# Kernel tuning notes

Hardware: AMD Instinct MI355X
Metric: run time of the kernel (lower is better)

## Reference

```python
import jax, jax.numpy as jnp
import numpy as np

B, L, F_DIM, H = 4, 384, 640, 128
K_COULOMB = 332.0
DIELECTRIC = 80.0
BN_EPS = 1e-5

# amino-acid charge table, index order 'ACDEFGHIKLMNPQRSTVWY'
_AA = 'ACDEFGHIKLMNPQRSTVWY'
_CHG = {'D': -1.0, 'E': -1.0, 'K': 1.0, 'R': 1.0, 'H': 0.1}
_TABLE = np.zeros((20, 3), dtype=np.float32)
for _i, _aa in enumerate(_AA):
    c = _CHG.get(_aa, 0.0)
    _TABLE[_i, 0 if c > 0 else (1 if c < 0 else 2)] = 1.0
CHG_TABLE = jnp.asarray(_TABLE)


def _conv1d(x, w, b, pad):
    # x: [N, Cin, L], w: [Cout, Cin, K]
    y = jax.lax.conv_general_dilated(x, w, (1,), [(pad, pad)],
                                     dimension_numbers=('NCH', 'OIH', 'NCH'))
    return y + b[None, :, None]


def setup_inputs() -> dict:
    key = jax.random.key(0)
    ks = jax.random.split(key, 32)
    s = 0.05

    def rn(k, shape):
        return (jax.random.normal(k, shape) * s).astype(jnp.float32)

    inp = {
        'features': jax.random.normal(ks[0], (B, L, F_DIM), dtype=jnp.float32),
        'seq_ids': jax.random.randint(ks[1], (B, L), 0, 20, dtype=jnp.int32),
        'structures': (jax.random.normal(ks[2], (B, L, 3)) * 10.0).astype(jnp.float32),
        # charge predictor: Linear(F,H) -> ReLU -> BN(H) -> Linear(H,H//2) -> ReLU -> Linear(H//2,3) -> Softmax
        'W1': rn(ks[3], (F_DIM, H)), 'b1': jnp.zeros((H,), jnp.float32),
        'gamma': jnp.ones((H,), jnp.float32), 'beta': jnp.zeros((H,), jnp.float32),
        'rmean': jnp.zeros((H,), jnp.float32), 'rvar': jnp.ones((H,), jnp.float32),
        'W2': rn(ks[4], (H, H // 2)), 'b2': jnp.zeros((H // 2,), jnp.float32),
        'W3': rn(ks[5], (H // 2, 3)), 'b3': jnp.zeros((3,), jnp.float32),
        # salt bridge detector: Linear(2F+1,H) -> ReLU -> Linear(H,64) -> ReLU -> Linear(64,1) -> Sigmoid
        'sW1': rn(ks[6], (2 * F_DIM + 1, H)), 'sb1': jnp.zeros((H,), jnp.float32),
        'sW2': rn(ks[7], (H, 64)), 'sb2': jnp.zeros((64,), jnp.float32),
        'sW3': rn(ks[8], (64, 1)), 'sb3': jnp.zeros((1,), jnp.float32),
        # potential calculator convs (OIH layout)
        'c1w': rn(ks[9], (16, 1, 5)), 'c1b': jnp.zeros((16,), jnp.float32),
        'c2w': rn(ks[10], (8, 16, 3)), 'c2b': jnp.zeros((8,), jnp.float32),
        'c3w': rn(ks[11], (1, 8, 3)), 'c3b': jnp.zeros((1,), jnp.float32),
    }
    return inp


def reference(features, seq_ids, structures,
              W1, b1, gamma, beta, rmean, rvar, W2, b2, W3, b3,
              sW1, sb1, sW2, sb2, sW3, sb3,
              c1w, c1b, c2w, c2b, c3w, c3b):
    b_, l_, f_ = features.shape

    # true charges from sequence (one-hot pos/neg/neutral)
    true_charges = CHG_TABLE[seq_ids]                               # [B,L,3]

    # --- charge predictor (BatchNorm in eval mode: running stats) ---
    x = features.reshape(-1, f_)
    h = jax.nn.relu(x @ W1 + b1)
    h = gamma * (h - rmean) / jnp.sqrt(rvar + BN_EPS) + beta
    h = jax.nn.relu(h @ W2 + b2)
    pc = jax.nn.softmax(h @ W3 + b3, axis=-1).reshape(b_, l_, 3)    # [B,L,3]

    net_charge = pc[:, :, 0:1] - pc[:, :, 1:2]                      # [B,L,1]

    # --- electrostatic potential: 1D conv stack on [B,1,L] ---
    p = net_charge.transpose(0, 2, 1)                               # [B,1,L]
    p = jax.nn.relu(_conv1d(p, c1w, c1b, 2))
    p = jax.nn.relu(_conv1d(p, c2w, c2b, 1))
    p = _conv1d(p, c3w, c3b, 1)
    potential = p.transpose(0, 2, 1)                                # [B,L,1]

    # --- pairwise distances ---
    diff = structures[:, :, None, :] - structures[:, None, :, :]    # [B,L,L,3]
    D = jnp.sqrt(jnp.sum(diff * diff, axis=-1) + 1e-12)             # [B,L,L]

    # --- salt bridges: vectorized edge-MLP over all (pos i, neg j) pairs ---
    pos = pc[:, :, 0] > pc[:, :, 2]                                 # [B,L]
    neg = pc[:, :, 1] > pc[:, :, 2]                                 # [B,L]
    a, bb, d = sW1[:f_], sW1[f_:2 * f_], sW1[2 * f_]                # split cat([fi,fj,dist]) @ sW1
    fi = features @ a                                               # [B,L,H]
    fj = features @ bb                                              # [B,L,H]
    hid = jax.nn.relu(fi[:, :, None, :] + fj[:, None, :, :] + D[..., None] * d + sb1)  # [B,L,L,H]
    hid2 = jax.nn.relu(hid @ sW2 + sb2)                             # [B,L,L,64]
    prob = jax.nn.sigmoid((hid2 @ sW3 + sb3)[..., 0])               # [B,L,L]
    q = pos[:, :, None] & neg[:, None, :] & (D < 4.0) & (prob > 0.5)
    salt_bridge_masks = (q | q.transpose(0, 2, 1)).astype(jnp.float32)  # [B,L,L]

    # --- Coulomb energy with distance-dependent dielectric ---
    # dielectric = eps * D / 4 -> e_ij = k * q_i q_j / (eps/4 * D^2)
    qc = pc[:, :, 0] - pc[:, :, 1]                                  # [B,L]
    valid = (D < 15.0) & (D > 0.0)
    triu = jnp.triu(jnp.ones((l_, l_), bool), k=1)[None]
    D_safe = jnp.where(valid, D, 1.0)
    e_ij = K_COULOMB * qc[:, :, None] * qc[:, None, :] / ((DIELECTRIC / 4.0) * D_safe * D_safe)
    energy = jnp.sum(jnp.where(valid & triu, e_ij, 0.0), axis=(1, 2))  # [B]

    return (pc, true_charges, net_charge, potential, salt_bridge_masks, energy)
```

## Files before the change

### kernel.cpp

```cpp
#include <hip/hip_runtime.h>

#define LSEQ 384
#define NROWS 1536
#define FDIM 640
#define HDIM 128
#define PART 196608

#define WS_H1   0
#define WS_FI   393216
#define WS_FJ   786432
#define WS_QC   1179648
#define WS_FLAG 1181184
#define WS_CNT  1182720
#define WS_LIST 1182724
#define CAPMAX  65536

#define OUT_PC    0
#define OUT_TC    4608
#define OUT_NET   9216
#define OUT_POT   10752
#define OUT_MASK  12288
#define OUT_EN    602112

__global__ __launch_bounds__(256) void k_gemm(const float* __restrict__ X,
                                              const float* __restrict__ W1,
                                              const float* __restrict__ sW1,
                                              float* __restrict__ ws) {
    __shared__ float As[32][34];
    __shared__ float Bs[32][64];
    const int t  = threadIdx.x;
    const int m0 = blockIdx.x * 32;
    const int gy = blockIdx.y;
    const int kz = blockIdx.z;
    const int mat = gy >> 1, half = gy & 1, n0 = half * 64;
    const float* W = (mat == 0) ? W1 : (mat == 1 ? sW1 : sW1 + 640 * 128);
    float* O = ws + (mat == 0 ? WS_H1 : (mat == 1 ? WS_FI : WS_FJ)) + kz * PART;

    const int a_r = t >> 3;
    const int a_c = (t & 7) * 4;
    const int b_r = t >> 4;
    const int b_c = (t & 15) * 4;
    const int tx  = (t & 15) * 4;
    const int ty  = (t >> 4) * 2;

    float acc[2][4] = {};
    const int k0 = kz * 320;

    for (int kk = k0; kk < k0 + 320; kk += 32) {
        float4 av = *(const float4*)&X[(m0 + a_r) * FDIM + kk + a_c];
        As[a_c + 0][a_r] = av.x;
        As[a_c + 1][a_r] = av.y;
        As[a_c + 2][a_r] = av.z;
        As[a_c + 3][a_r] = av.w;
        *(float4*)&Bs[b_r][b_c]      = *(const float4*)&W[(kk + b_r) * HDIM + n0 + b_c];
        *(float4*)&Bs[b_r + 16][b_c] = *(const float4*)&W[(kk + b_r + 16) * HDIM + n0 + b_c];
        __syncthreads();
#pragma unroll
        for (int k = 0; k < 32; k++) {
            float2 a = *(const float2*)&As[k][ty];
            float4 b = *(const float4*)&Bs[k][tx];
            acc[0][0] = fmaf(a.x, b.x, acc[0][0]);
            acc[0][1] = fmaf(a.x, b.y, acc[0][1]);
            acc[0][2] = fmaf(a.x, b.z, acc[0][2]);
            acc[0][3] = fmaf(a.x, b.w, acc[0][3]);
            acc[1][0] = fmaf(a.y, b.x, acc[1][0]);
            acc[1][1] = fmaf(a.y, b.y, acc[1][1]);
            acc[1][2] = fmaf(a.y, b.z, acc[1][2]);
            acc[1][3] = fmaf(a.y, b.w, acc[1][3]);
        }
        __syncthreads();
    }
#pragma unroll
    for (int r = 0; r < 2; r++) {
        float4 v = make_float4(acc[r][0], acc[r][1], acc[r][2], acc[r][3]);
        *(float4*)&O[(m0 + ty + r) * HDIM + n0 + tx] = v;
    }
}

__global__ __launch_bounds__(256) void k_row(const float* __restrict__ h1a,
                                             const float* __restrict__ h1b,
                                             const float* __restrict__ b1,
                                             const float* __restrict__ gam,
                                             const float* __restrict__ bet,
                                             const float* __restrict__ rmean,
                                             const float* __restrict__ rvar,
                                             const float* __restrict__ W2,
                                             const float* __restrict__ b2,
                                             const float* __restrict__ W3,
                                             const float* __restrict__ b3,
                                             const int* __restrict__ seq,
                                             float* __restrict__ out,
                                             float* __restrict__ qc,
                                             int* __restrict__ flags) {
    __shared__ float sh[4][130];
    const int t = threadIdx.x, w = t >> 6, lane = t & 63;
    const int row = blockIdx.x * 4 + w;
#pragma unroll
    for (int c = lane; c < 128; c += 64) {
        float v = h1a[row * HDIM + c] + h1b[row * HDIM + c] + b1[c];
        v = fmaxf(v, 0.0f);
        v = gam[c] * (v - rmean[c]) / sqrtf(rvar[c] + 1e-5f) + bet[c];
        sh[w][c] = v;
    }
    __syncthreads();
    float acc = b2[lane];
#pragma unroll 8
    for (int c = 0; c < 128; c++)
        acc = fmaf(sh[w][c], W2[c * 64 + lane], acc);
    float h2 = fmaxf(acc, 0.0f);
    float x0 = h2 * W3[lane * 3 + 0];
    float x1 = h2 * W3[lane * 3 + 1];
    float x2 = h2 * W3[lane * 3 + 2];
#pragma unroll
    for (int o = 32; o > 0; o >>= 1) {
        x0 += __shfl_xor(x0, o, 64);
        x1 += __shfl_xor(x1, o, 64);
        x2 += __shfl_xor(x2, o, 64);
    }
    if (lane == 0) {
        float l0 = x0 + b3[0], l1 = x1 + b3[1], l2 = x2 + b3[2];
        float m = fmaxf(l0, fmaxf(l1, l2));
        float e0 = expf(l0 - m), e1 = expf(l1 - m), e2 = expf(l2 - m);
        float s = e0 + e1 + e2;
        float pc0 = e0 / s, pc1 = e1 / s, pc2 = e2 / s;
        out[OUT_PC + row * 3 + 0] = pc0;
        out[OUT_PC + row * 3 + 1] = pc1;
        out[OUT_PC + row * 3 + 2] = pc2;
        float net = pc0 - pc1;
        out[OUT_NET + row] = net;
        qc[row] = net;
        flags[row] = (pc0 > pc2 ? 1 : 0) | (pc1 > pc2 ? 2 : 0);
        int sid = seq[row];
        float c0 = (sid == 6 || sid == 8 || sid == 14) ? 1.0f : 0.0f;
        float c1 = (sid == 2 || sid == 3) ? 1.0f : 0.0f;
        out[OUT_TC + row * 3 + 0] = c0;
        out[OUT_TC + row * 3 + 1] = c1;
        out[OUT_TC + row * 3 + 2] = (c0 == 0.0f && c1 == 0.0f) ? 1.0f : 0.0f;
    }
}

__global__ __launch_bounds__(384) void k_conv(const float* __restrict__ net,
                                              const float* __restrict__ c1w, const float* __restrict__ c1b,
                                              const float* __restrict__ c2w, const float* __restrict__ c2b,
                                              const float* __restrict__ c3w, const float* __restrict__ c3b,
                                              float* __restrict__ out,
                                              unsigned int* __restrict__ cnt) {
    __shared__ float p0[LSEQ + 4];
    __shared__ float p1[16][LSEQ + 2];
    __shared__ float p2[8][LSEQ + 2];
    const int b = blockIdx.x, t = threadIdx.x;
    p0[t + 2] = net[b * LSEQ + t];
    if (t < 2) { p0[t] = 0.0f; p0[LSEQ + 2 + t] = 0.0f; }
    if (t < 16) { p1[t][0] = 0.0f; p1[t][LSEQ + 1] = 0.0f; }
    if (t < 8)  { p2[t][0] = 0.0f; p2[t][LSEQ + 1] = 0.0f; }
    if (b == 0) {
        if (t < 4) out[OUT_EN + t] = 0.0f;
        if (t == 4) *cnt = 0u;
    }
    __syncthreads();
#pragma unroll
    for (int o = 0; o < 16; o++) {
        float acc = c1b[o];
#pragma unroll
        for (int k = 0; k < 5; k++) acc = fmaf(p0[t + k], c1w[o * 5 + k], acc);
        p1[o][t + 1] = fmaxf(acc, 0.0f);
    }
    __syncthreads();
#pragma unroll
    for (int o = 0; o < 8; o++) {
        float acc = c2b[o];
        for (int i = 0; i < 16; i++)
#pragma unroll
            for (int k = 0; k < 3; k++)
                acc = fmaf(p1[i][t + k], c2w[(o * 16 + i) * 3 + k], acc);
        p2[o][t + 1] = fmaxf(acc, 0.0f);
    }
    __syncthreads();
    {
        float acc = c3b[0];
        for (int i = 0; i < 8; i++)
#pragma unroll
            for (int k = 0; k < 3; k++)
                acc = fmaf(p2[i][t + k], c3w[i * 3 + k], acc);
        out[OUT_POT + b * LSEQ + t] = acc;
    }
}

__global__ __launch_bounds__(256) void k_pair(const float* __restrict__ S,
                                              const float* __restrict__ qc,
                                              const int* __restrict__ flags,
                                              float* __restrict__ out,
                                              unsigned int* __restrict__ cnt,
                                              unsigned int* __restrict__ list,
                                              unsigned int cap) {
    __shared__ float sx[LSEQ], sy[LSEQ], sz[LSEQ], sq[LSEQ];
    __shared__ int sf[LSEQ];
    __shared__ float red[4];
    const int row = blockIdx.x;
    const int b = row / LSEQ;
    const int i = row - b * LSEQ;
    const int t = threadIdx.x;
    for (int j = t; j < LSEQ; j += 256) {
        int g = b * LSEQ + j;
        sx[j] = S[g * 3 + 0];
        sy[j] = S[g * 3 + 1];
        sz[j] = S[g * 3 + 2];
        sq[j] = qc[g];
        sf[j] = flags[g];
    }
    __syncthreads();
    const float six = sx[i], siy = sy[i], siz = sz[i], qi = sq[i];
    const bool posi = (sf[i] & 1) != 0;
    const int lane = t & 63;
    float esum = 0.0f;
    float* mrow = out + OUT_MASK + (long)row * LSEQ;
    for (int j = t; j < LSEQ; j += 256) {
        float dx = __fsub_rn(six, sx[j]);
        float dy = __fsub_rn(siy, sy[j]);
        float dz = __fsub_rn(siz, sz[j]);
        float d2 = __fadd_rn(__fadd_rn(__fmul_rn(dx, dx), __fmul_rn(dy, dy)), __fmul_rn(dz, dz));
        d2 = __fadd_rn(d2, 1e-12f);
        float D = __fsqrt_rn(d2);
        mrow[j] = 0.0f;
        if (j > i && D < 15.0f && D > 0.0f) {
            float num = __fmul_rn(__fmul_rn(332.0f, qi), sq[j]);
            float den = __fmul_rn(__fmul_rn(20.0f, D), D);
            esum += __fdiv_rn(num, den);
        }
        bool cand = posi && ((sf[j] & 2) != 0) && (D < 4.0f);
        unsigned long long mball = __ballot(cand);
        int nc = __popcll(mball);
        unsigned int base = 0;
        if (lane == 0 && nc > 0) base = atomicAdd(cnt, (unsigned int)nc);
        base = __shfl(base, 0, 64);
        if (cand) {
            int off = __popcll(mball & ((1ull << lane) - 1ull));
            unsigned int p = base + (unsigned int)off;
            if (p < cap) list[p] = ((unsigned int)row << 9) | (unsigned int)j;
        }
    }
    for (int o = 32; o > 0; o >>= 1) esum += __shfl_xor(esum, o, 64);
    if (lane == 0) red[t >> 6] = esum;
    __syncthreads();
    if (t == 0) {
        float s = red[0] + red[1] + red[2] + red[3];
        atomicAdd(&out[OUT_EN + b], s);
    }
}

__global__ __launch_bounds__(256) void k_cand(const float* __restrict__ S,
                                              const float* __restrict__ fiA,
                                              const float* __restrict__ fiB,
                                              const float* __restrict__ fjA,
                                              const float* __restrict__ fjB,
                                              const float* __restrict__ sW1,
                                              const float* __restrict__ sb1,
                                              const float* __restrict__ sW2,
                                              const float* __restrict__ sb2,
                                              const float* __restrict__ sW3,
                                              const float* __restrict__ sb3,
                                              const unsigned int* __restrict__ cnt,
                                              const unsigned int* __restrict__ list,
                                              float* __restrict__ out,
                                              unsigned int cap) {
    unsigned int n = *cnt;
    if (n > cap) n = cap;
    if (blockIdx.x * 4 >= n) return;

    __shared__ float w2s[128 * 64];
    const int t = threadIdx.x;
    for (int idx = t; idx < 2048; idx += 256)
        ((float4*)w2s)[idx] = ((const float4*)sW2)[idx];

    const int lane = t & 63;
    const int w = t >> 6;
    const float* dvec = sW1 + 1280 * 128;
    const float dv0 = dvec[lane],    dv1 = dvec[lane + 64];
    const float sb0 = sb1[lane],     sb1v = sb1[lane + 64];
    const float w3  = sW3[lane];
    const float b2v = sb2[lane];
    const float b3v = sb3[0];
    float* mask = out + OUT_MASK;
    __syncthreads();

    const int gw = blockIdx.x * 4 + w;
    const int nw = gridDim.x * 4;
    for (unsigned int c = (unsigned int)gw; c < n; c += (unsigned int)nw) {
        unsigned int v = list[c];
        int row = (int)(v >> 9);
        int j = (int)(v & 511u);
        int i = row % LSEQ;
        int col = row - i + j;
        float dx = __fsub_rn(S[row * 3 + 0], S[col * 3 + 0]);
        float dy = __fsub_rn(S[row * 3 + 1], S[col * 3 + 1]);
        float dz = __fsub_rn(S[row * 3 + 2], S[col * 3 + 2]);
        float d2 = __fadd_rn(__fadd_rn(__fmul_rn(dx, dx), __fmul_rn(dy, dy)), __fmul_rn(dz, dz));
        d2 = __fadd_rn(d2, 1e-12f);
        float D = __fsqrt_rn(d2);
        float fi0 = fiA[(long)row * 128 + lane]      + fiB[(long)row * 128 + lane];
        float fi1 = fiA[(long)row * 128 + 64 + lane] + fiB[(long)row * 128 + 64 + lane];
        float fj0 = fjA[(long)col * 128 + lane]      + fjB[(long)col * 128 + lane];
        float fj1 = fjA[(long)col * 128 + 64 + lane] + fjB[(long)col * 128 + 64 + lane];
        float h0 = fmaxf(fi0 + fj0 + D * dv0 + sb0, 0.0f);
        float h1 = fmaxf(fi1 + fj1 + D * dv1 + sb1v, 0.0f);
        float acc0 = 0.0f, acc1 = 0.0f;
#pragma unroll
        for (int cc = 0; cc < 64; cc++) {
            float hv0 = __uint_as_float(__builtin_amdgcn_readlane(__float_as_uint(h0), cc));
            float hv1 = __uint_as_float(__builtin_amdgcn_readlane(__float_as_uint(h1), cc));
            acc0 = fmaf(hv0, w2s[cc * 64 + lane], acc0);
            acc1 = fmaf(hv1, w2s[(cc + 64) * 64 + lane], acc1);
        }
        float x = fmaxf(acc0 + acc1 + b2v, 0.0f) * w3;
        for (int o = 32; o > 0; o >>= 1) x += __shfl_xor(x, o, 64);
        if (lane == 0 && (x + b3v) > 0.0f) {
            mask[(long)row * LSEQ + j] = 1.0f;
            mask[(long)col * LSEQ + i] = 1.0f;
        }
    }
}

extern "C" void kernel_launch(void* const* d_in, const int* in_sizes, int n_in,
                              void* d_out, int out_size, void* d_ws, size_t ws_size,
                              hipStream_t stream) {
    const float* X     = (const float*)d_in[0];
    const int*   seq   = (const int*)d_in[1];
    const float* S     = (const float*)d_in[2];
    const float* W1    = (const float*)d_in[3];
    const float* b1    = (const float*)d_in[4];
    const float* gam   = (const float*)d_in[5];
    const float* bet   = (const float*)d_in[6];
    const float* rmean = (const float*)d_in[7];
    const float* rvar  = (const float*)d_in[8];
    const float* W2    = (const float*)d_in[9];
    const float* b2    = (const float*)d_in[10];
    const float* W3    = (const float*)d_in[11];
    const float* b3    = (const float*)d_in[12];
    const float* sW1   = (const float*)d_in[13];
    const float* sb1   = (const float*)d_in[14];
    const float* sW2   = (const float*)d_in[15];
    const float* sb2   = (const float*)d_in[16];
    const float* sW3   = (const float*)d_in[17];
    const float* sb3   = (const float*)d_in[18];
    const float* c1w   = (const float*)d_in[19];
    const float* c1b   = (const float*)d_in[20];
    const float* c2w   = (const float*)d_in[21];
    const float* c2b   = (const float*)d_in[22];
    const float* c3w   = (const float*)d_in[23];
    const float* c3b   = (const float*)d_in[24];

    float* out = (float*)d_out;
    float* ws  = (float*)d_ws;
    unsigned int* cnt  = (unsigned int*)(ws + WS_CNT);
    unsigned int* list = (unsigned int*)(ws + WS_LIST);
    int* flags = (int*)(ws + WS_FLAG);

    unsigned int cap = 0;
    size_t ws_floats = ws_size / 4;
    if (ws_floats > (size_t)WS_LIST) {
        size_t room = ws_floats - WS_LIST;
        cap = (unsigned int)(room < CAPMAX ? room : CAPMAX);
    }

    hipLaunchKernelGGL(k_gemm, dim3(48, 6, 2), dim3(256), 0, stream, X, W1, sW1, ws);
    hipLaunchKernelGGL(k_row, dim3(384), dim3(256), 0, stream,
                       ws + WS_H1, ws + WS_H1 + PART, b1, gam, bet, rmean, rvar,
                       W2, b2, W3, b3, seq, out, ws + WS_QC, flags);
    hipLaunchKernelGGL(k_conv, dim3(4), dim3(384), 0, stream,
                       out + OUT_NET, c1w, c1b, c2w, c2b, c3w, c3b, out, cnt);
    hipLaunchKernelGGL(k_pair, dim3(1536), dim3(256), 0, stream,
                       S, ws + WS_QC, flags, out, cnt, list, cap);
    hipLaunchKernelGGL(k_cand, dim3(192), dim3(256), 0, stream,
                       S, ws + WS_FI, ws + WS_FI + PART, ws + WS_FJ, ws + WS_FJ + PART,
                       sW1, sb1, sW2, sb2, sW3, sb3, cnt, list, out, cap);
}
```

Before: 190.0 us.

## Fuse five kernels into two with per-row candidate MLP evaluation

Merges the charge-predictor GEMM with its BN/MLP/softmax epilogue in the same blocks, and runs the salt-bridge GEMMs as extra blocks of that launch. Conv, pairwise energy and candidate MLP evaluation share a second launch, where each row block keeps a local candidate list in shared memory instead of a global atomic list. This is meant to remove launch gaps, the global split-K round trip for the first layer, and the separate candidate kernel. In exchange, row blocks that find candidates each reload the sW2 table, and each block writes only its own row of the mask, evaluating both pair directions.

Result: faster. 171.5 us (-9.7%).

```diff
diff --git a/kernel.cpp b/kernel.cpp
--- a/kernel.cpp
+++ b/kernel.cpp
@@ -6,14 +6,10 @@
 #define HDIM 128
 #define PART 196608
 
-#define WS_H1   0
-#define WS_FI   393216
-#define WS_FJ   786432
-#define WS_QC   1179648
-#define WS_FLAG 1181184
-#define WS_CNT  1182720
-#define WS_LIST 1182724
-#define CAPMAX  65536
+#define WS_FI   0
+#define WS_FJ   393216
+#define WS_QC   786432
+#define WS_FLAG 787968
 
 #define OUT_PC    0
 #define OUT_TC    4608
@@ -22,198 +18,307 @@
 #define OUT_MASK  12288
 #define OUT_EN    602112
 
-__global__ __launch_bounds__(256) void k_gemm(const float* __restrict__ X,
-                                              const float* __restrict__ W1,
-                                              const float* __restrict__ sW1,
-                                              float* __restrict__ ws) {
-    __shared__ float As[32][34];
-    __shared__ float Bs[32][64];
-    const int t  = threadIdx.x;
-    const int m0 = blockIdx.x * 32;
-    const int gy = blockIdx.y;
-    const int kz = blockIdx.z;
-    const int mat = gy >> 1, half = gy & 1, n0 = half * 64;
-    const float* W = (mat == 0) ? W1 : (mat == 1 ? sW1 : sW1 + 640 * 128);
-    float* O = ws + (mat == 0 ? WS_H1 : (mat == 1 ? WS_FI : WS_FJ)) + kz * PART;
-
-    const int a_r = t >> 3;
-    const int a_c = (t & 7) * 4;
-    const int b_r = t >> 4;
-    const int b_c = (t & 15) * 4;
-    const int tx  = (t & 15) * 4;
-    const int ty  = (t >> 4) * 2;
-
-    float acc[2][4] = {};
-    const int k0 = kz * 320;
-
-    for (int kk = k0; kk < k0 + 320; kk += 32) {
-        float4 av = *(const float4*)&X[(m0 + a_r) * FDIM + kk + a_c];
-        As[a_c + 0][a_r] = av.x;
-        As[a_c + 1][a_r] = av.y;
-        As[a_c + 2][a_r] = av.z;
-        As[a_c + 3][a_r] = av.w;
-        *(float4*)&Bs[b_r][b_c]      = *(const float4*)&W[(kk + b_r) * HDIM + n0 + b_c];
-        *(float4*)&Bs[b_r + 16][b_c] = *(const float4*)&W[(kk + b_r + 16) * HDIM + n0 + b_c];
+__global__ __launch_bounds__(256) void k1(const float* __restrict__ X,
+                                          const float* __restrict__ W1,
+                                          const float* __restrict__ sW1,
+                                          const float* __restrict__ b1,
+                                          const float* __restrict__ gam,
+                                          const float* __restrict__ bet,
+                                          const float* __restrict__ rmean,
+                                          const float* __restrict__ rvar,
+                                          const float* __restrict__ W2,
+                                          const float* __restrict__ b2,
+                                          const float* __restrict__ W3,
+                                          const float* __restrict__ b3,
+                                          const int* __restrict__ seq,
+                                          float* __restrict__ out,
+                                          float* __restrict__ ws) {
+    __shared__ char smem[27648];
+    const int t = threadIdx.x;
+    const int blk = blockIdx.x;
+
+    if (blk == 0 && t < 4) out[OUT_EN + t] = 0.0f;
+
+    if (blk < 96) {
+        float* As = (float*)smem;
+        float* Bs = (float*)(smem + 2304);
+        float* hs = (float*)(smem + 18688);
+        const int m0 = blk * 16;
+        const int tx = (t & 31) * 4;
+        const int ty = (t >> 5) * 2;
+        float acc[2][4] = {};
+        for (int kk = 0; kk < FDIM; kk += 32) {
+            if (t < 128) {
+                int a_r = t >> 3, a_c = (t & 7) * 4;
+                float4 av = *(const float4*)&X[(m0 + a_r) * FDIM + kk + a_c];
+                As[(a_c + 0) * 18 + a_r] = av.x;
+                As[(a_c + 1) * 18 + a_r] = av.y;
+                As[(a_c + 2) * 18 + a_r] = av.z;
+                As[(a_c + 3) * 18 + a_r] = av.w;
+            }
+#pragma unroll
+            for (int q = 0; q < 4; q++) {
+                int idx = t + 256 * q;
+                int r = idx >> 5, c4 = (idx & 31) * 4;
+                *(float4*)&Bs[r * 128 + c4] = *(const float4*)&W1[(kk + r) * HDIM + c4];
+            }
+            __syncthreads();
+#pragma unroll
+            for (int k = 0; k < 32; k++) {
+                float2 a = *(const float2*)&As[k * 18 + ty];
+                float4 b = *(const float4*)&Bs[k * 128 + tx];
+                acc[0][0] = fmaf(a.x, b.x, acc[0][0]);
+                acc[0][1] = fmaf(a.x, b.y, acc[0][1]);
+                acc[0][2] = fmaf(a.x, b.z, acc[0][2]);
+                acc[0][3] = fmaf(a.x, b.w, acc[0][3]);
+                acc[1][0] = fmaf(a.y, b.x, acc[1][0]);
+                acc[1][1] = fmaf(a.y, b.y, acc[1][1]);
+                acc[1][2] = fmaf(a.y, b.z, acc[1][2]);
+                acc[1][3] = fmaf(a.y, b.w, acc[1][3]);
+            }
+            __syncthreads();
+        }
+        {
+            float4 b1v = *(const float4*)&b1[tx];
+            float4 g4  = *(const float4*)&gam[tx];
+            float4 be4 = *(const float4*)&bet[tx];
+            float4 rm4 = *(const float4*)&rmean[tx];
+            float4 rv4 = *(const float4*)&rvar[tx];
+            float rs0 = 1.0f / sqrtf(rv4.x + 1e-5f);
+            float rs1 = 1.0f / sqrtf(rv4.y + 1e-5f);
+            float rs2 = 1.0f / sqrtf(rv4.z + 1e-5f);
+            float rs3 = 1.0f / sqrtf(rv4.w + 1e-5f);
+#pragma unroll
+            for (int r = 0; r < 2; r++) {
+                float v0 = g4.x * (fmaxf(acc[r][0] + b1v.x, 0.0f) - rm4.x) * rs0 + be4.x;
+                float v1 = g4.y * (fmaxf(acc[r][1] + b1v.y, 0.0f) - rm4.y) * rs1 + be4.y;
+                float v2 = g4.z * (fmaxf(acc[r][2] + b1v.z, 0.0f) - rm4.z) * rs2 + be4.z;
+                float v3 = g4.w * (fmaxf(acc[r][3] + b1v.w, 0.0f) - rm4.w) * rs3 + be4.w;
+                *(float4*)&hs[(ty + r) * 132 + tx] = make_float4(v0, v1, v2, v3);
+            }
+        }
         __syncthreads();
-#pragma unroll
-        for (int k = 0; k < 32; k++) {
-            float2 a = *(const float2*)&As[k][ty];
-            float4 b = *(const float4*)&Bs[k][tx];
-            acc[0][0] = fmaf(a.x, b.x, acc[0][0]);
-            acc[0][1] = fmaf(a.x, b.y, acc[0][1]);
-            acc[0][2] = fmaf(a.x, b.z, acc[0][2]);
-            acc[0][3] = fmaf(a.x, b.w, acc[0][3]);
-            acc[1][0] = fmaf(a.y, b.x, acc[1][0]);
-            acc[1][1] = fmaf(a.y, b.y, acc[1][1]);
-            acc[1][2] = fmaf(a.y, b.z, acc[1][2]);
-            acc[1][3] = fmaf(a.y, b.w, acc[1][3]);
-        }
+        const int w = t >> 6, lane = t & 63;
+        float h0r[4], h1r[4], acc2[4];
+#pragma unroll
+        for (int r = 0; r < 4; r++) {
+            h0r[r] = hs[(w * 4 + r) * 132 + lane];
+            h1r[r] = hs[(w * 4 + r) * 132 + 64 + lane];
+            acc2[r] = b2[lane];
+        }
+#pragma unroll
+        for (int cc = 0; cc < 64; cc++) {
+            float wv0 = W2[cc * 64 + lane];
+            float wv1 = W2[(cc + 64) * 64 + lane];
+#pragma unroll
+            for (int r = 0; r < 4; r++) {
+                float hv0 = __uint_as_float(__builtin_amdgcn_readlane(__float_as_uint(h0r[r]), cc));
+                float hv1 = __uint_as_float(__builtin_amdgcn_readlane(__float_as_uint(h1r[r]), cc));
+                acc2[r] = fmaf(hv0, wv0, acc2[r]);
+                acc2[r] = fmaf(hv1, wv1, acc2[r]);
+            }
+        }
+        float w30 = W3[lane * 3 + 0], w31 = W3[lane * 3 + 1], w32 = W3[lane * 3 + 2];
+#pragma unroll
+        for (int r = 0; r < 4; r++) {
+            float h2 = fmaxf(acc2[r], 0.0f);
+            float x0 = h2 * w30, x1 = h2 * w31, x2 = h2 * w32;
+#pragma unroll
+            for (int o = 32; o > 0; o >>= 1) {
+                x0 += __shfl_xor(x0, o, 64);
+                x1 += __shfl_xor(x1, o, 64);
+                x2 += __shfl_xor(x2, o, 64);
+            }
+            if (lane == 0) {
+                int row = m0 + w * 4 + r;
+                float l0 = x0 + b3[0], l1 = x1 + b3[1], l2 = x2 + b3[2];
+                float m = fmaxf(l0, fmaxf(l1, l2));
+                float e0 = expf(l0 - m), e1 = expf(l1 - m), e2 = expf(l2 - m);
+                float s = e0 + e1 + e2;
+                float pc0 = e0 / s, pc1 = e1 / s, pc2 = e2 / s;
+                out[OUT_PC + row * 3 + 0] = pc0;
+                out[OUT_PC + row * 3 + 1] = pc1;
+                out[OUT_PC + row * 3 + 2] = pc2;
+                float net = pc0 - pc1;
+                out[OUT_NET + row] = net;
+                ws[WS_QC + row] = net;
+                ((int*)(ws + WS_FLAG))[row] = (pc0 > pc2 ? 1 : 0) | (pc1 > pc2 ? 2 : 0);
+                int sid = seq[row];
+                float c0 = (sid == 6 || sid == 8 || sid == 14) ? 1.0f : 0.0f;
+                float c1 = (sid == 2 || sid == 3) ? 1.0f : 0.0f;
+                out[OUT_TC + row * 3 + 0] = c0;
+                out[OUT_TC + row * 3 + 1] = c1;
+                out[OUT_TC + row * 3 + 2] = (c0 == 0.0f && c1 == 0.0f) ? 1.0f : 0.0f;
+            }
+        }
+    } else {
+        float* As = (float*)smem;
+        float* Bs = (float*)(smem + 4352);
+        const int bi = blk - 96;
+        const int kz = bi & 1, half = (bi >> 1) & 1, mat = (bi >> 2) & 1, mt = bi >> 3;
+        const int m0 = mt * 32, n0 = half * 64;
+        const float* W = sW1 + mat * 640 * 128;
+        float* O = ws + (mat == 0 ? WS_FI : WS_FJ) + kz * PART;
+        const int a_r = t >> 3, a_c = (t & 7) * 4;
+        const int b_r = t >> 4, b_c = (t & 15) * 4;
+        const int tx = (t & 15) * 4, ty = (t >> 4) * 2;
+        float acc[2][4] = {};
+        const int k0 = kz * 320;
+        for (int kk = k0; kk < k0 + 320; kk += 32) {
+            float4 av = *(const float4*)&X[(m0 + a_r) * FDIM + kk + a_c];
+            As[(a_c + 0) * 34 + a_r] = av.x;
+            As[(a_c + 1) * 34 + a_r] = av.y;
+            As[(a_c + 2) * 34 + a_r] = av.z;
+            As[(a_c + 3) * 34 + a_r] = av.w;
+            *(float4*)&Bs[b_r * 64 + b_c]        = *(const float4*)&W[(kk + b_r) * HDIM + n0 + b_c];
+            *(float4*)&Bs[(b_r + 16) * 64 + b_c] = *(const float4*)&W[(kk + b_r + 16) * HDIM + n0 + b_c];
+            __syncthreads();
+#pragma unroll
+            for (int k = 0; k < 32; k++) {
+                float2 a = *(const float2*)&As[k * 34 + ty];
+                float4 b = *(const float4*)&Bs[k * 64 + tx];
+                acc[0][0] = fmaf(a.x, b.x, acc[0][0]);
+                acc[0][1] = fmaf(a.x, b.y, acc[0][1]);
+                acc[0][2] = fmaf(a.x, b.z, acc[0][2]);
+                acc[0][3] = fmaf(a.x, b.w, acc[0][3]);
+                acc[1][0] = fmaf(a.y, b.x, acc[1][0]);
+                acc[1][1] = fmaf(a.y, b.y, acc[1][1]);
+                acc[1][2] = fmaf(a.y, b.z, acc[1][2]);
+                acc[1][3] = fmaf(a.y, b.w, acc[1][3]);
+            }
+            __syncthreads();
+        }
+#pragma unroll
+        for (int r = 0; r < 2; r++) {
+            float4 v = make_float4(acc[r][0], acc[r][1], acc[r][2], acc[r][3]);
+            *(float4*)&O[(m0 + ty + r) * HDIM + n0 + tx] = v;
+        }
+    }
+}
+
+__device__ __forceinline__ float mlp_eval(const float* __restrict__ fiA, const float* __restrict__ fiB,
+                                          const float* __restrict__ fjA, const float* __restrict__ fjB,
+                                          int gi, int gj, float D,
+                                          float dv0, float dv1, float sb0, float sb1v,
+                                          float b2v, float w3l, const float* w2s, int lane) {
+    float fi0 = fiA[gi * 128 + lane]      + fiB[gi * 128 + lane];
+    float fi1 = fiA[gi * 128 + 64 + lane] + fiB[gi * 128 + 64 + lane];
+    float fj0 = fjA[gj * 128 + lane]      + fjB[gj * 128 + lane];
+    float fj1 = fjA[gj * 128 + 64 + lane] + fjB[gj * 128 + 64 + lane];
+    float h0 = fmaxf(fi0 + fj0 + D * dv0 + sb0, 0.0f);
+    float h1 = fmaxf(fi1 + fj1 + D * dv1 + sb1v, 0.0f);
+    float a0 = 0.0f, a1 = 0.0f;
+#pragma unroll
+    for (int cc = 0; cc < 64; cc++) {
+        float hv0 = __uint_as_float(__builtin_amdgcn_readlane(__float_as_uint(h0), cc));
+        float hv1 = __uint_as_float(__builtin_amdgcn_readlane(__float_as_uint(h1), cc));
+        a0 = fmaf(hv0, w2s[cc * 64 + lane], a0);
+        a1 = fmaf(hv1, w2s[(cc + 64) * 64 + lane], a1);
+    }
+    float x = fmaxf(a0 + a1 + b2v, 0.0f) * w3l;
+#pragma unroll
+    for (int o = 32; o > 0; o >>= 1) x += __shfl_xor(x, o, 64);
+    return x;
+}
+
+__global__ __launch_bounds__(256) void k2(const float* __restrict__ S,
+                                          const float* __restrict__ ws,
+                                          const float* __restrict__ sW1,
+                                          const float* __restrict__ sb1,
+                                          const float* __restrict__ sW2,
+                                          const float* __restrict__ sb2,
+                                          const float* __restrict__ sW3,
+                                          const float* __restrict__ sb3,
+                                          const float* __restrict__ c1w, const float* __restrict__ c1b,
+                                          const float* __restrict__ c2w, const float* __restrict__ c2b,
+                                          const float* __restrict__ c3w, const float* __restrict__ c3b,
+                                          float* __restrict__ out) {
+    __shared__ char smem[40960];
+    const int t = threadIdx.x;
+    const int bi = blockIdx.x;
+
+    if (bi < 4) {
+        float* p0 = (float*)smem;
+        float* p1 = p0 + 388;
+        float* p2 = p1 + 16 * 386;
+        const int b = bi;
+        for (int j = t; j < LSEQ; j += 256) p0[j + 2] = out[OUT_NET + b * LSEQ + j];
+        if (t < 2) { p0[t] = 0.0f; p0[LSEQ + 2 + t] = 0.0f; }
+        if (t < 16) { p1[t * 386] = 0.0f; p1[t * 386 + 385] = 0.0f; }
+        if (t < 8)  { p2[t * 386] = 0.0f; p2[t * 386 + 385] = 0.0f; }
         __syncthreads();
-    }
-#pragma unroll
-    for (int r = 0; r < 2; r++) {
-        float4 v = make_float4(acc[r][0], acc[r][1], acc[r][2], acc[r][3]);
-        *(float4*)&O[(m0 + ty + r) * HDIM + n0 + tx] = v;
-    }
-}
-
-__global__ __launch_bounds__(256) void k_row(const float* __restrict__ h1a,
-                                             const float* __restrict__ h1b,
-                                             const float* __restrict__ b1,
-                                             const float* __restrict__ gam,
-                                             const float* __restrict__ bet,
-                                             const float* __restrict__ rmean,
-                                             const float* __restrict__ rvar,
-                                             const float* __restrict__ W2,
-                                             const float* __restrict__ b2,
-                                             const float* __restrict__ W3,
-                                             const float* __restrict__ b3,
-                                             const int* __restrict__ seq,
-                                             float* __restrict__ out,
-                                             float* __restrict__ qc,
-                                             int* __restrict__ flags) {
-    __shared__ float sh[4][130];
-    const int t = threadIdx.x, w = t >> 6, lane = t & 63;
-    const int row = blockIdx.x * 4 + w;
-#pragma unroll
-    for (int c = lane; c < 128; c += 64) {
-        float v = h1a[row * HDIM + c] + h1b[row * HDIM + c] + b1[c];
-        v = fmaxf(v, 0.0f);
-        v = gam[c] * (v - rmean[c]) / sqrtf(rvar[c] + 1e-5f) + bet[c];
-        sh[w][c] = v;
-    }
-    __syncthreads();
-    float acc = b2[lane];
-#pragma unroll 8
-    for (int c = 0; c < 128; c++)
-        acc = fmaf(sh[w][c], W2[c * 64 + lane], acc);
-    float h2 = fmaxf(acc, 0.0f);
-    float x0 = h2 * W3[lane * 3 + 0];
-    float x1 = h2 * W3[lane * 3 + 1];
-    float x2 = h2 * W3[lane * 3 + 2];
-#pragma unroll
-    for (int o = 32; o > 0; o >>= 1) {
-        x0 += __shfl_xor(x0, o, 64);
-        x1 += __shfl_xor(x1, o, 64);
-        x2 += __shfl_xor(x2, o, 64);
-    }
-    if (lane == 0) {
-        float l0 = x0 + b3[0], l1 = x1 + b3[1], l2 = x2 + b3[2];
-        float m = fmaxf(l0, fmaxf(l1, l2));
-        float e0 = expf(l0 - m), e1 = expf(l1 - m), e2 = expf(l2 - m);
-        float s = e0 + e1 + e2;
-        float pc0 = e0 / s, pc1 = e1 / s, pc2 = e2 / s;
-        out[OUT_PC + row * 3 + 0] = pc0;
-        out[OUT_PC + row * 3 + 1] = pc1;
-        out[OUT_PC + row * 3 + 2] = pc2;
-        float net = pc0 - pc1;
-        out[OUT_NET + row] = net;
-        qc[row] = net;
-        flags[row] = (pc0 > pc2 ? 1 : 0) | (pc1 > pc2 ? 2 : 0);
-        int sid = seq[row];
-        float c0 = (sid == 6 || sid == 8 || sid == 14) ? 1.0f : 0.0f;
-        float c1 = (sid == 2 || sid == 3) ? 1.0f : 0.0f;
-        out[OUT_TC + row * 3 + 0] = c0;
-        out[OUT_TC + row * 3 + 1] = c1;
-        out[OUT_TC + row * 3 + 2] = (c0 == 0.0f && c1 == 0.0f) ? 1.0f : 0.0f;
-    }
-}
-
-__global__ __launch_bounds__(384) void k_conv(const float* __restrict__ net,
-                                              const float* __restrict__ c1w, const float* __restrict__ c1b,
-                                              const float* __restrict__ c2w, const float* __restrict__ c2b,
-                                              const float* __restrict__ c3w, const float* __restrict__ c3b,
-                                              float* __restrict__ out,
-                                              unsigned int* __restrict__ cnt) {
-    __shared__ float p0[LSEQ + 4];
-    __shared__ float p1[16][LSEQ + 2];
-    __shared__ float p2[8][LSEQ + 2];
-    const int b = blockIdx.x, t = threadIdx.x;
-    p0[t + 2] = net[b * LSEQ + t];
-    if (t < 2) { p0[t] = 0.0f; p0[LSEQ + 2 + t] = 0.0f; }
-    if (t < 16) { p1[t][0] = 0.0f; p1[t][LSEQ + 1] = 0.0f; }
-    if (t < 8)  { p2[t][0] = 0.0f; p2[t][LSEQ + 1] = 0.0f; }
-    if (b == 0) {
-        if (t < 4) out[OUT_EN + t] = 0.0f;
-        if (t == 4) *cnt = 0u;
-    }
-    __syncthreads();
-#pragma unroll
-    for (int o = 0; o < 16; o++) {
-        float acc = c1b[o];
-#pragma unroll
-        for (int k = 0; k < 5; k++) acc = fmaf(p0[t + k], c1w[o * 5 + k], acc);
-        p1[o][t + 1] = fmaxf(acc, 0.0f);
-    }
-    __syncthreads();
-#pragma unroll
-    for (int o = 0; o < 8; o++) {
-        float acc = c2b[o];
-        for (int i = 0; i < 16; i++)
-#pragma unroll
-            for (int k = 0; k < 3; k++)
-                acc = fmaf(p1[i][t + k], c2w[(o * 16 + i) * 3 + k], acc);
-        p2[o][t + 1] = fmaxf(acc, 0.0f);
-    }
-    __syncthreads();
-    {
-        float acc = c3b[0];
-        for (int i = 0; i < 8; i++)
-#pragma unroll
-            for (int k = 0; k < 3; k++)
-                acc = fmaf(p2[i][t + k], c3w[i * 3 + k], acc);
-        out[OUT_POT + b * LSEQ + t] = acc;
-    }
-}
-
-__global__ __launch_bounds__(256) void k_pair(const float* __restrict__ S,
-                                              const float* __restrict__ qc,
-                                              const int* __restrict__ flags,
-                                              float* __restrict__ out,
-                                              unsigned int* __restrict__ cnt,
-                                              unsigned int* __restrict__ list,
-                                              unsigned int cap) {
-    __shared__ float sx[LSEQ], sy[LSEQ], sz[LSEQ], sq[LSEQ];
-    __shared__ int sf[LSEQ];
-    __shared__ float red[4];
-    const int row = blockIdx.x;
+        for (int pos = t; pos < LSEQ; pos += 256) {
+#pragma unroll
+            for (int o = 0; o < 16; o++) {
+                float acc = c1b[o];
+#pragma unroll
+                for (int k = 0; k < 5; k++) acc = fmaf(p0[pos + k], c1w[o * 5 + k], acc);
+                p1[o * 386 + pos + 1] = fmaxf(acc, 0.0f);
+            }
+        }
+        __syncthreads();
+        for (int pos = t; pos < LSEQ; pos += 256) {
+#pragma unroll
+            for (int o = 0; o < 8; o++) {
+                float acc = c2b[o];
+                for (int i = 0; i < 16; i++)
+#pragma unroll
+                    for (int k = 0; k < 3; k++)
+                        acc = fmaf(p1[i * 386 + pos + k], c2w[(o * 16 + i) * 3 + k], acc);
+                p2[o * 386 + pos + 1] = fmaxf(acc, 0.0f);
+            }
+        }
+        __syncthreads();
+        for (int pos = t; pos < LSEQ; pos += 256) {
+            float acc = c3b[0];
+            for (int i = 0; i < 8; i++)
+#pragma unroll
+                for (int k = 0; k < 3; k++)
+                    acc = fmaf(p2[i * 386 + pos + k], c3w[i * 3 + k], acc);
+            out[OUT_POT + b * LSEQ + pos] = acc;
+        }
+        return;
+    }
+
+    float* sx = (float*)smem;
+    float* sy = sx + 384;
+    float* sz = sy + 384;
+    float* sq = sz + 384;
+    unsigned int* clist = (unsigned int*)(sz + 768);
+    unsigned char* sf = (unsigned char*)(smem + 7680);
+    float* red = (float*)(smem + 8064);
+    int* cntL = (int*)(smem + 8080);
+    float* w2s = (float*)(smem + 8192);
+
+    const float* qc = ws + WS_QC;
+    const int* flags = (const int*)(ws + WS_FLAG);
+    const float* fiA = ws + WS_FI;
+    const float* fiB = ws + WS_FI + PART;
+    const float* fjA = ws + WS_FJ;
+    const float* fjB = ws + WS_FJ + PART;
+
+    const int row = bi - 4;
     const int b = row / LSEQ;
     const int i = row - b * LSEQ;
-    const int t = threadIdx.x;
+
     for (int j = t; j < LSEQ; j += 256) {
         int g = b * LSEQ + j;
         sx[j] = S[g * 3 + 0];
         sy[j] = S[g * 3 + 1];
         sz[j] = S[g * 3 + 2];
         sq[j] = qc[g];
-        sf[j] = flags[g];
-    }
+        sf[j] = (unsigned char)flags[g];
+    }
+    if (t == 0) *cntL = 0;
     __syncthreads();
+
     const float six = sx[i], siy = sy[i], siz = sz[i], qi = sq[i];
-    const bool posi = (sf[i] & 1) != 0;
-    const int lane = t & 63;
+    const int fli = sf[i];
+    const bool posi = (fli & 1) != 0, negi = (fli & 2) != 0;
+    const int lane = t & 63, w = t >> 6;
     float esum = 0.0f;
     float* mrow = out + OUT_MASK + (long)row * LSEQ;
+
     for (int j = t; j < LSEQ; j += 256) {
         float dx = __fsub_rn(six, sx[j]);
         float dy = __fsub_rn(siy, sy[j]);
@@ -227,96 +332,58 @@
             float den = __fmul_rn(__fmul_rn(20.0f, D), D);
             esum += __fdiv_rn(num, den);
         }
-        bool cand = posi && ((sf[j] & 2) != 0) && (D < 4.0f);
-        unsigned long long mball = __ballot(cand);
-        int nc = __popcll(mball);
-        unsigned int base = 0;
-        if (lane == 0 && nc > 0) base = atomicAdd(cnt, (unsigned int)nc);
-        base = __shfl(base, 0, 64);
-        if (cand) {
-            int off = __popcll(mball & ((1ull << lane) - 1ull));
-            unsigned int p = base + (unsigned int)off;
-            if (p < cap) list[p] = ((unsigned int)row << 9) | (unsigned int)j;
-        }
-    }
+        int flj = sf[j];
+        bool near = (D < 4.0f);
+        bool need1 = near && posi && ((flj & 2) != 0);
+        bool need2 = near && negi && ((flj & 1) != 0);
+        if (need1 || need2) {
+            int p = atomicAdd(cntL, 1);
+            clist[p] = (unsigned int)j | (need1 ? 512u : 0u) | (need2 ? 1024u : 0u);
+        }
+    }
+#pragma unroll
     for (int o = 32; o > 0; o >>= 1) esum += __shfl_xor(esum, o, 64);
-    if (lane == 0) red[t >> 6] = esum;
+    if (lane == 0) red[w] = esum;
     __syncthreads();
     if (t == 0) {
         float s = red[0] + red[1] + red[2] + red[3];
         atomicAdd(&out[OUT_EN + b], s);
     }
-}
-
-__global__ __launch_bounds__(256) void k_cand(const float* __restrict__ S,
-                                              const float* __restrict__ fiA,
-                                              const float* __restrict__ fiB,
-                                              const float* __restrict__ fjA,
-                                              const float* __restrict__ fjB,
-                                              const float* __restrict__ sW1,
-                                              const float* __restrict__ sb1,
-                                              const float* __restrict__ sW2,
-                                              const float* __restrict__ sb2,
-                                              const float* __restrict__ sW3,
-                                              const float* __restrict__ sb3,
-                                              const unsigned int* __restrict__ cnt,
-                                              const unsigned int* __restrict__ list,
-                                              float* __restrict__ out,
-                                              unsigned int cap) {
-    unsigned int n = *cnt;
-    if (n > cap) n = cap;
-    if (blockIdx.x * 4 >= n) return;
-
-    __shared__ float w2s[128 * 64];
-    const int t = threadIdx.x;
+
+    int nc = *cntL;
+    if (nc == 0) return;
+
     for (int idx = t; idx < 2048; idx += 256)
         ((float4*)w2s)[idx] = ((const float4*)sW2)[idx];
-
-    const int lane = t & 63;
-    const int w = t >> 6;
     const float* dvec = sW1 + 1280 * 128;
-    const float dv0 = dvec[lane],    dv1 = dvec[lane + 64];
-    const float sb0 = sb1[lane],     sb1v = sb1[lane + 64];
-    const float w3  = sW3[lane];
+    const float dv0 = dvec[lane], dv1 = dvec[lane + 64];
+    const float sb0 = sb1[lane], sb1v = sb1[lane + 64];
+    const float w3l = sW3[lane];
     const float b2v = sb2[lane];
     const float b3v = sb3[0];
-    float* mask = out + OUT_MASK;
     __syncthreads();
 
-    const int gw = blockIdx.x * 4 + w;
-    const int nw = gridDim.x * 4;
-    for (unsigned int c = (unsigned int)gw; c < n; c += (unsigned int)nw) {
-        unsigned int v = list[c];
-        int row = (int)(v >> 9);
-        int j = (int)(v & 511u);
-        int i = row % LSEQ;
-        int col = row - i + j;
-        float dx = __fsub_rn(S[row * 3 + 0], S[col * 3 + 0]);
-        float dy = __fsub_rn(S[row * 3 + 1], S[col * 3 + 1]);
-        float dz = __fsub_rn(S[row * 3 + 2], S[col * 3 + 2]);
+    for (int c = w; c < nc; c += 4) {
+        unsigned int e = clist[c];
+        int j = (int)(e & 511u);
+        bool need1 = (e & 512u) != 0, need2 = (e & 1024u) != 0;
+        float dx = __fsub_rn(six, sx[j]);
+        float dy = __fsub_rn(siy, sy[j]);
+        float dz = __fsub_rn(siz, sz[j]);
         float d2 = __fadd_rn(__fadd_rn(__fmul_rn(dx, dx), __fmul_rn(dy, dy)), __fmul_rn(dz, dz));
         d2 = __fadd_rn(d2, 1e-12f);
         float D = __fsqrt_rn(d2);
-        float fi0 = fiA[(long)row * 128 + lane]      + fiB[(long)row * 128 + lane];
-        float fi1 = fiA[(long)row * 128 + 64 + lane] + fiB[(long)row * 128 + 64 + lane];
-        float fj0 = fjA[(long)col * 128 + lane]      + fjB[(long)col * 128 + lane];
-        float fj1 = fjA[(long)col * 128 + 64 + lane] + fjB[(long)col * 128 + 64 + lane];
-        float h0 = fmaxf(fi0 + fj0 + D * dv0 + sb0, 0.0f);
-        float h1 = fmaxf(fi1 + fj1 + D * dv1 + sb1v, 0.0f);
-        float acc0 = 0.0f, acc1 = 0.0f;
-#pragma unroll
-        for (int cc = 0; cc < 64; cc++) {
-            float hv0 = __uint_as_float(__builtin_amdgcn_readlane(__float_as_uint(h0), cc));
-            float hv1 = __uint_as_float(__builtin_amdgcn_readlane(__float_as_uint(h1), cc));
-            acc0 = fmaf(hv0, w2s[cc * 64 + lane], acc0);
-            acc1 = fmaf(hv1, w2s[(cc + 64) * 64 + lane], acc1);
-        }
-        float x = fmaxf(acc0 + acc1 + b2v, 0.0f) * w3;
-        for (int o = 32; o > 0; o >>= 1) x += __shfl_xor(x, o, 64);
-        if (lane == 0 && (x + b3v) > 0.0f) {
-            mask[(long)row * LSEQ + j] = 1.0f;
-            mask[(long)col * LSEQ + i] = 1.0f;
-        }
+        int gi = row, gj = b * LSEQ + j;
+        bool hit = false;
+        if (need1) {
+            float x = mlp_eval(fiA, fiB, fjA, fjB, gi, gj, D, dv0, dv1, sb0, sb1v, b2v, w3l, w2s, lane);
+            hit = (x + b3v) > 0.0f;
+        }
+        if (!hit && need2) {
+            float x = mlp_eval(fiA, fiB, fjA, fjB, gj, gi, D, dv0, dv1, sb0, sb1v, b2v, w3l, w2s, lane);
+            hit = (x + b3v) > 0.0f;
+        }
+        if (hit && lane == 0) mrow[j] = 1.0f;
     }
 }
 
@@ -351,26 +418,11 @@
 
     float* out = (float*)d_out;
     float* ws  = (float*)d_ws;
-    unsigned int* cnt  = (unsigned int*)(ws + WS_CNT);
-    unsigned int* list = (unsigned int*)(ws + WS_LIST);
-    int* flags = (int*)(ws + WS_FLAG);
-
-    unsigned int cap = 0;
-    size_t ws_floats = ws_size / 4;
-    if (ws_floats > (size_t)WS_LIST) {
-        size_t room = ws_floats - WS_LIST;
-        cap = (unsigned int)(room < CAPMAX ? room : CAPMAX);
-    }
-
-    hipLaunchKernelGGL(k_gemm, dim3(48, 6, 2), dim3(256), 0, stream, X, W1, sW1, ws);
-    hipLaunchKernelGGL(k_row, dim3(384), dim3(256), 0, stream,
-                       ws + WS_H1, ws + WS_H1 + PART, b1, gam, bet, rmean, rvar,
-                       W2, b2, W3, b3, seq, out, ws + WS_QC, flags);
-    hipLaunchKernelGGL(k_conv, dim3(4), dim3(384), 0, stream,
-                       out + OUT_NET, c1w, c1b, c2w, c2b, c3w, c3b, out, cnt);
-    hipLaunchKernelGGL(k_pair, dim3(1536), dim3(256), 0, stream,
-                       S, ws + WS_QC, flags, out, cnt, list, cap);
-    hipLaunchKernelGGL(k_cand, dim3(192), dim3(256), 0, stream,
-                       S, ws + WS_FI, ws + WS_FI + PART, ws + WS_FJ, ws + WS_FJ + PART,
-                       sW1, sb1, sW2, sb2, sW3, sb3, cnt, list, out, cap);
+
+    hipLaunchKernelGGL(k1, dim3(480), dim3(256), 0, stream,
+                       X, W1, sW1, b1, gam, bet, rmean, rvar, W2, b2, W3, b3,
+                       seq, out, ws);
+    hipLaunchKernelGGL(k2, dim3(1540), dim3(256), 0, stream,
+                       S, ws, sW1, sb1, sW2, sb2, sW3, sb3,
+                       c1w, c1b, c2w, c2b, c3w, c3b, out);
 }
```
